# Optimization experiments

Measured on AMD Instinct MI355X. Metric: run time of the kernel, lower is better.

## Reference

```python
import jax, jax.numpy as jnp
import numpy as np

B, T, C, H = 2, 2048, 1024, 16


def setup_inputs() -> dict:
    key = jax.random.key(0)
    ks = jax.random.split(key, 9)
    s = 1.0 / np.sqrt(C)
    return {
        "query": jax.random.normal(ks[0], (B, T, C), dtype=jnp.float32),
        "Wq": jax.random.normal(ks[1], (C, C), dtype=jnp.float32) * s,
        "bq": jnp.zeros((C,), dtype=jnp.float32),
        "Wk": jax.random.normal(ks[2], (C, C), dtype=jnp.float32) * s,
        "bk": jnp.zeros((C,), dtype=jnp.float32),
        "Wv": jax.random.normal(ks[3], (C, C), dtype=jnp.float32) * s,
        "bv": jnp.zeros((C,), dtype=jnp.float32),
        "Wp": jax.random.normal(ks[4], (C, C), dtype=jnp.float32) * s,
        "bp": jnp.zeros((C,), dtype=jnp.float32),
        "n_head": H,
    }


def reference(query, Wq, bq, Wk, bk, Wv, bv, Wp, bp, n_head):
    b, t, c = query.shape
    d = c // n_head
    # QKV projections -> [b, h, t, d]
    q = (query @ Wq + bq).reshape(b, t, n_head, d).transpose(0, 2, 1, 3)
    k = (query @ Wk + bk).reshape(b, t, n_head, d).transpose(0, 2, 1, 3)
    v = (query @ Wv + bv).reshape(b, t, n_head, d).transpose(0, 2, 1, 3)
    scale = 1.0 / jnp.sqrt(jnp.asarray(d, dtype=query.dtype))
    att = jnp.einsum('bhtd,bhsd->bhts', q, k) * scale  # [b,h,t,t]
    causal = jnp.tril(jnp.ones((t, t), dtype=bool))
    att = jnp.where(causal[None, None, :, :], att, -jnp.inf)
    att = jax.nn.softmax(att, axis=-1)
    y = jnp.einsum('bhts,bhsd->bhtd', att, v)  # [b,h,t,d]
    y = y.transpose(0, 2, 1, 3).reshape(b, t, c)
    return y @ Wp + bp
```

## Files before the change

### kernel.cpp

```cpp
#include <hip/hip_runtime.h>
#include <math.h>

#define B_ 2
#define T_ 2048
#define C_ 1024
#define H_ 16
#define D_ 64
#define M_ (B_*T_)

typedef __bf16 bf16x8 __attribute__((ext_vector_type(8)));
typedef __bf16 bf16x4 __attribute__((ext_vector_type(4)));
typedef float  f32x4  __attribute__((ext_vector_type(4)));
typedef float  f32x16 __attribute__((ext_vector_type(16)));

__device__ __forceinline__ unsigned short f2bf(float f) {
    unsigned int u = __float_as_uint(f);
    u += 0x7FFFu + ((u >> 16) & 1u);
    return (unsigned short)(u >> 16);
}

__device__ __forceinline__ bf16x8 pack4(unsigned a, unsigned b,
                                        unsigned c, unsigned d) {
    union { unsigned u[4]; bf16x8 v; } t;
    t.u[0] = a; t.u[1] = b; t.u[2] = c; t.u[3] = d;
    return t.v;
}

__device__ __forceinline__ void gload16(const void* g, void* l) {
    __builtin_amdgcn_global_load_lds(
        (const __attribute__((address_space(1))) void*)g,
        (__attribute__((address_space(3))) void*)l, 16, 0, 0);
}

__global__ __launch_bounds__(256) void prep_kernel(
    const float* __restrict__ X, unsigned short* __restrict__ Xb,
    const float* __restrict__ W0, const float* __restrict__ W1,
    const float* __restrict__ W2, const float* __restrict__ W3,
    unsigned short* __restrict__ T0, unsigned short* __restrict__ T1,
    unsigned short* __restrict__ T2, unsigned short* __restrict__ T3)
{
    const int tid = threadIdx.x;
    if (blockIdx.x < 2048) {
        const size_t i = ((size_t)blockIdx.x * 256 + tid) * 8;
        const float4 a = *(const float4*)&X[i];
        const float4 b = *(const float4*)&X[i + 4];
        ushort4 s0, s1;
        s0.x = f2bf(a.x); s0.y = f2bf(a.y); s0.z = f2bf(a.z); s0.w = f2bf(a.w);
        s1.x = f2bf(b.x); s1.y = f2bf(b.y); s1.z = f2bf(b.z); s1.w = f2bf(b.w);
        *(ushort4*)&Xb[i]     = s0;
        *(ushort4*)&Xb[i + 4] = s1;
        return;
    }
    const int bz = blockIdx.x - 2048;
    const int z = bz >> 10, rem = bz & 1023;
    const float* W; unsigned short* Wt;
    switch (z) {
        case 0: W = W0; Wt = T0; break;
        case 1: W = W1; Wt = T1; break;
        case 2: W = W2; Wt = T2; break;
        default: W = W3; Wt = T3; break;
    }
    __shared__ unsigned short tile[32][33];
    const int k0 = (rem >> 5) * 32, n0 = (rem & 31) * 32;
    {
        const int r = tid >> 3, c = (tid & 7) * 4;
        const float4 v = *(const float4*)&W[(size_t)(k0 + r)*C_ + n0 + c];
        tile[c+0][r] = f2bf(v.x);
        tile[c+1][r] = f2bf(v.y);
        tile[c+2][r] = f2bf(v.z);
        tile[c+3][r] = f2bf(v.w);
    }
    __syncthreads();
    {
        const int r = tid >> 3, c = (tid & 7) * 4;
        ushort4 s;
        s.x = tile[r][c+0]; s.y = tile[r][c+1]; s.z = tile[r][c+2]; s.w = tile[r][c+3];
        *(ushort4*)&Wt[(size_t)(n0 + r)*C_ + k0 + c] = s;
    }
}

__global__ __launch_bounds__(256) void gemm_proj_kernel(
    const unsigned short* __restrict__ A, const unsigned short* __restrict__ Bt,
    const float* __restrict__ bias, float* __restrict__ out)
{
    __shared__ __align__(16) unsigned short lds[4 * 6144];

    const int tid  = threadIdx.x;
    const int lane = tid & 63;
    const int wave = tid >> 6;
    const int wm = wave >> 1, wn = wave & 1;
    const int l15 = lane & 15, quad = lane >> 4;
    const int m0 = blockIdx.y * 64, n0 = blockIdx.x * 128;

    const int lrow = lane >> 2;
    const int csw  = ((lane & 3) ^ ((lane >> 3) & 3)) * 8;
    const int sw8  = (quad ^ ((l15 >> 1) & 3)) * 8;

#define PSTAGE(tt) do {                                                        \
        const int bi_ = ((tt) & 3) * 6144;                                     \
        const int k0_ = (tt) << 5;                                             \
        gload16(&A [(size_t)(m0 + wave*16 + lrow)*C_ + k0_ + csw],             \
                &lds[bi_ + wave*512]);                                         \
        gload16(&Bt[(size_t)(n0 + wave*32 + lrow)*C_ + k0_ + csw],             \
                &lds[bi_ + 2048 + wave*1024]);                                 \
        gload16(&Bt[(size_t)(n0 + wave*32 + 16 + lrow)*C_ + k0_ + csw],        \
                &lds[bi_ + 2048 + wave*1024 + 512]);                           \
    } while (0)

    const f32x4 zero4 = {0.f, 0.f, 0.f, 0.f};
    f32x4 acc[2][4];
    #pragma unroll
    for (int i = 0; i < 2; ++i)
        #pragma unroll
        for (int j = 0; j < 4; ++j) acc[i][j] = zero4;

    PSTAGE(0); PSTAGE(1); PSTAGE(2);

    for (int t = 0; t < 32; ++t) {
        const int bi = (t & 3) * 6144;
        __builtin_amdgcn_s_barrier();
        __builtin_amdgcn_sched_barrier(0);
        if (t <= 29) {
            asm volatile("s_waitcnt vmcnt(6)" ::: "memory");
        } else if (t == 30) {
            asm volatile("s_waitcnt vmcnt(3)" ::: "memory");
        } else {
            asm volatile("s_waitcnt vmcnt(0)" ::: "memory");
        }
        __builtin_amdgcn_s_barrier();
        __builtin_amdgcn_sched_barrier(0);

        const unsigned short* Ab = &lds[bi];
        const unsigned short* Bb = &lds[bi + 2048];

        bf16x8 af[2], bfr[4];
        #pragma unroll
        for (int i = 0; i < 2; ++i)
            af[i] = *(const bf16x8*)&Ab[(wm*32 + i*16 + l15)*32 + sw8];
        #pragma unroll
        for (int j = 0; j < 4; ++j)
            bfr[j] = *(const bf16x8*)&Bb[(wn*64 + j*16 + l15)*32 + sw8];

        if (t < 29) PSTAGE(t + 3);

        __builtin_amdgcn_s_setprio(1);
        #pragma unroll
        for (int i = 0; i < 2; ++i)
            #pragma unroll
            for (int j = 0; j < 4; ++j)
                acc[i][j] = __builtin_amdgcn_mfma_f32_16x16x32_bf16(
                    af[i], bfr[j], acc[i][j], 0, 0, 0);
        __builtin_amdgcn_s_setprio(0);
    }
#undef PSTAGE

    #pragma unroll
    for (int j = 0; j < 4; ++j) {
        const int n = n0 + wn*64 + j*16 + l15;
        const float bv = bias[n];
        #pragma unroll
        for (int i = 0; i < 2; ++i)
            #pragma unroll
            for (int r = 0; r < 4; ++r) {
                const int m = m0 + wm*32 + i*16 + quad*4 + r;
                out[(size_t)m*C_ + n] = acc[i][j][r] + bv;
            }
    }
}

__global__ __launch_bounds__(512, 2) void gemm256_qkv_kernel(
    const unsigned short* __restrict__ A, const unsigned short* __restrict__ Bt,
    const float* __restrict__ b0, const float* __restrict__ b1,
    const float* __restrict__ b2,
    unsigned short* __restrict__ outq, unsigned short* __restrict__ outk,
    unsigned short* __restrict__ outv)
{
    __shared__ __align__(16) unsigned short lds[4 * 16384];

    const int tid  = threadIdx.x;
    const int lane = tid & 63;
    const int wave = tid >> 6;
    const int l15  = lane & 15, quad = lane >> 4;
    const int wm   = wave >> 2, wn = wave & 3;
    const int bid  = blockIdx.y * 12 + blockIdx.x;
    const int swz  = (bid & 7) * 24 + (bid >> 3);
    const int m0   = (swz / 12) * 256, n0 = (swz % 12) * 256;

    const int lrow = lane >> 2;
    const int csw  = ((lane & 3) ^ ((lane >> 3) & 3)) * 8;
    const int sw8  = (quad ^ ((l15 >> 1) & 3)) * 8;

#define STAGE_H(tt, h) do {                                                    \
        const int bi_ = ((tt) & 3) << 14;                                      \
        const int k0_ = (tt) << 5;                                             \
        const int ra_ = m0 + wave*32 + (h)*16 + lrow;                          \
        const int rb_ = n0 + wave*32 + (h)*16 + lrow;                          \
        gload16(&A [(size_t)ra_*C_ + k0_ + csw],                               \
                &lds[bi_ + wave*1024 + (h)*512]);                              \
        gload16(&Bt[(size_t)rb_*C_ + k0_ + csw],                               \
                &lds[bi_ + 8192 + wave*1024 + (h)*512]);                       \
    } while (0)

    const f32x4 zero4 = {0.f, 0.f, 0.f, 0.f};
    f32x4 acc[8][4];
    #pragma unroll
    for (int i = 0; i < 8; ++i)
        #pragma unroll
        for (int j = 0; j < 4; ++j) acc[i][j] = zero4;

    STAGE_H(0,0); STAGE_H(0,1);
    STAGE_H(1,0); STAGE_H(1,1);
    STAGE_H(2,0); STAGE_H(2,1);

    for (int t = 0; t < 32; ++t) {
        const int bi = (t & 3) << 14;
        __builtin_amdgcn_s_barrier();
        __builtin_amdgcn_sched_barrier(0);
        if (t <= 29) {
            asm volatile("s_waitcnt vmcnt(8)" ::: "memory");
        } else if (t == 30) {
            asm volatile("s_waitcnt vmcnt(4)" ::: "memory");
        } else {
            asm volatile("s_waitcnt vmcnt(0)" ::: "memory");
        }
        __builtin_amdgcn_s_barrier();
        __builtin_amdgcn_sched_barrier(0);

        const unsigned short* Ab = &lds[bi];
        const unsigned short* Bb = &lds[bi + 8192];

        bf16x8 bfr[4], af[4];
        #pragma unroll
        for (int j = 0; j < 4; ++j)
            bfr[j] = *(const bf16x8*)&Bb[(wn*64 + j*16 + l15)*32 + sw8];
        #pragma unroll
        for (int i = 0; i < 4; ++i)
            af[i] = *(const bf16x8*)&Ab[(wm*128 + i*16 + l15)*32 + sw8];

        if (t < 29) STAGE_H(t + 3, 0);

        __builtin_amdgcn_s_setprio(1);
        #pragma unroll
        for (int i = 0; i < 4; ++i)
            #pragma unroll
            for (int j = 0; j < 4; ++j)
                acc[i][j] = __builtin_amdgcn_mfma_f32_16x16x32_bf16(
                    af[i], bfr[j], acc[i][j], 0, 0, 0);
        __builtin_amdgcn_s_setprio(0);

        __builtin_amdgcn_s_barrier();
        __builtin_amdgcn_sched_barrier(0);

        #pragma unroll
        for (int i = 0; i < 4; ++i)
            af[i] = *(const bf16x8*)&Ab[(wm*128 + 64 + i*16 + l15)*32 + sw8];

        if (t < 29) STAGE_H(t + 3, 1);

        __builtin_amdgcn_s_setprio(1);
        #pragma unroll
        for (int i = 0; i < 4; ++i)
            #pragma unroll
            for (int j = 0; j < 4; ++j)
                acc[4+i][j] = __builtin_amdgcn_mfma_f32_16x16x32_bf16(
                    af[i], bfr[j], acc[4+i][j], 0, 0, 0);
        __builtin_amdgcn_s_setprio(0);
    }
#undef STAGE_H

    __syncthreads();

    unsigned short* Ep = &lds[wave * 8192];
    const int which = n0 >> 10;
    const int c0 = (n0 & 1023) + wn * 64;
    const int h  = c0 >> 6;
    const int bb = m0 >> 11;
    const int t0 = (m0 & (T_ - 1)) + wm * 128;
    const int bh = bb * H_ + h;
    const float* bp = (which == 0) ? b0 : (which == 1 ? b1 : b2);
    const float qscale = (which == 0) ? 0.18033688f : 1.0f;

    if (which < 2) {
        __bf16* Eb = (__bf16*)Ep;
        #pragma unroll
        for (int j = 0; j < 4; ++j) {
            const int cl = j*16 + l15;
            const float bias = bp[c0 + cl];
            #pragma unroll
            for (int i = 0; i < 8; ++i)
                #pragma unroll
                for (int r = 0; r < 4; ++r)
                    Eb[(i*16 + quad*4 + r)*64 + cl] =
                        (__bf16)((acc[i][j][r] + bias) * qscale);
        }
        unsigned short* op = (which == 0) ? outq : outk;
        const int row8 = lane >> 3, chunk = lane & 7;
        #pragma unroll
        for (int u = 0; u < 16; ++u) {
            const int row = u*8 + row8;
            const uint4 v = *(const uint4*)&Ep[row*64 + chunk*8];
            *(uint4*)&op[((size_t)bh*T_ + t0 + row)*D_ + chunk*8] = v;
        }
    } else {
        #pragma unroll
        for (int j = 0; j < 4; ++j) {
            const int cl = j*16 + l15;
            const float bias = bp[c0 + cl];
            const int xo = (cl & 7) * 8;
            #pragma unroll
            for (int i = 0; i < 8; ++i) {
                bf16x4 pk = {(__bf16)(acc[i][j][0] + bias),
                             (__bf16)(acc[i][j][1] + bias),
                             (__bf16)(acc[i][j][2] + bias),
                             (__bf16)(acc[i][j][3] + bias)};
                *(bf16x4*)&Ep[cl*128 + ((i*16 + quad*4) ^ xo)] = pk;
            }
        }
        const int d4 = lane >> 4, chunk = lane & 15;
        #pragma unroll
        for (int u = 0; u < 16; ++u) {
            const int d = u*4 + d4;
            const uint4 v = *(const uint4*)&Ep[d*128 + ((chunk*8) ^ ((d & 7)*8))];
            *(uint4*)&outv[((size_t)bh*D_ + d)*T_ + t0 + chunk*8] = v;
        }
    }
}

__global__ __launch_bounds__(256) void flash_mfma_kernel(
    const unsigned short* __restrict__ Qs, const unsigned short* __restrict__ Ks,
    const unsigned short* __restrict__ Vts, unsigned short* __restrict__ Y,
    float* __restrict__ parts, float* __restrict__ lbase)
{
    __shared__ __align__(16) unsigned short Kls[64 * 64];
    __shared__ __align__(16) unsigned short Vls[64 * 64];
    __shared__ float lsums[4][32];

    const int tid  = threadIdx.x;
    const int lane = tid & 63, wave = tid >> 6;
    const int krl  = lane & 31, hi = lane >> 5;
    const int srow8 = lane >> 3;
    const int schk8 = ((lane & 7) ^ srow8) * 8;
    const int job  = blockIdx.x >> 5;
    const int bh   = blockIdx.x & 31;
    const bool isA = (job < 8);
    const int a    = isA ? job : job - 8;

    int qts[2], slos[2], shis[2], slots[2], nseg;
    if (isA) {
        qts[0] = a;      slos[0] = 0;        shis[0] = 2*a + 2;  slots[0] = -1;
        qts[1] = 15 - a; slos[1] = 0;        shis[1] = 15 - 2*a; slots[1] = 0;
        nseg = 2;
    } else {
        qts[0] = 15 - a; slos[0] = 15 - 2*a; shis[0] = 32 - 2*a; slots[0] = 1;
        nseg = 1;
    }

    const int b_ = bh >> 4, h_ = bh & (H_ - 1);

#define FSTAGE(itv) do {                                                       \
        const int s0_ = (itv) * 64;                                            \
        const int cu0_ = 2*wave, cu1_ = 2*wave + 1;                            \
        const int r0_ = cu0_*8 + srow8, r1_ = cu1_*8 + srow8;                  \
        gload16(&Ks [((size_t)bh*T_ + s0_ + r0_)*D_ + schk8],                  \
                (char*)Kls + cu0_*1024);                                       \
        gload16(&Vts[((size_t)bh*D_ + r0_)*T_ + s0_ + schk8],                  \
                (char*)Vls + cu0_*1024);                                       \
        gload16(&Ks [((size_t)bh*T_ + s0_ + r1_)*D_ + schk8],                  \
                (char*)Kls + cu1_*1024);                                       \
        gload16(&Vts[((size_t)bh*D_ + r1_)*T_ + s0_ + schk8],                  \
                (char*)Vls + cu1_*1024);                                       \
    } while (0)

    for (int sg = 0; sg < nseg; ++sg) {
        const int qt  = qts[sg];
        const int qw0 = qt * 128 + wave * 32;
        const int qrow = qw0 + krl;

        bf16x8 qf[4];
        #pragma unroll
        for (int ds = 0; ds < 4; ++ds)
            qf[ds] = *(const bf16x8*)&Qs[((size_t)bh*T_ + qrow)*D_ + ds*16 + hi*8];

        f32x16 o[2];
        #pragma unroll
        for (int dt = 0; dt < 2; ++dt)
            #pragma unroll
            for (int r = 0; r < 16; ++r) o[dt][r] = 0.f;
        float lsum = 0.f;

        for (int it = slos[sg]; it < shis[sg]; ++it) {
            const int s0 = it * 64;
            __syncthreads();
            FSTAGE(it);
            __syncthreads();

            if (s0 > qw0 + 31) continue;

            f32x16 st[2];
            #pragma unroll
            for (int kt = 0; kt < 2; ++kt)
                #pragma unroll
                for (int r = 0; r < 16; ++r) st[kt][r] = 0.f;
            #pragma unroll
            for (int kt = 0; kt < 2; ++kt) {
                #pragma unroll
                for (int ds = 0; ds < 4; ++ds) {
                    const int row = kt*32 + krl;
                    bf16x8 kf = *(const bf16x8*)
                        &Kls[row*64 + (((ds*2 + hi) ^ (krl & 7)) << 3)];
                    st[kt] = __builtin_amdgcn_mfma_f32_32x32x16_bf16(
                        kf, qf[ds], st[kt], 0, 0, 0);
                }
            }

            const bool diag = (s0 + 63 > qw0);
            #pragma unroll
            for (int kt = 0; kt < 2; ++kt) {
                const int kb = s0 + kt*32 + 4*hi;
                #pragma unroll
                for (int reg = 0; reg < 16; ++reg) {
                    const int crow = (reg & 3) + 8*(reg >> 2);
                    float e = __builtin_amdgcn_exp2f(st[kt][reg]);
                    if (diag && (kb + crow > qrow)) e = 0.f;
                    st[kt][reg] = e;
                    lsum += e;
                }
            }

            bf16x8 pa[4];
            #pragma unroll
            for (int kt = 0; kt < 2; ++kt) {
                #pragma unroll
                for (int hh = 0; hh < 2; ++hh) {
                    const int rb = hh * 8;
                    unsigned c0, c1, c2, c3;
                    asm("v_cvt_pk_bf16_f32 %0, %1, %2"
                        : "=v"(c0) : "v"(st[kt][rb+0]), "v"(st[kt][rb+1]));
                    asm("v_cvt_pk_bf16_f32 %0, %1, %2"
                        : "=v"(c1) : "v"(st[kt][rb+2]), "v"(st[kt][rb+3]));
                    asm("v_cvt_pk_bf16_f32 %0, %1, %2"
                        : "=v"(c2) : "v"(st[kt][rb+4]), "v"(st[kt][rb+5]));
                    asm("v_cvt_pk_bf16_f32 %0, %1, %2"
                        : "=v"(c3) : "v"(st[kt][rb+6]), "v"(st[kt][rb+7]));
                    asm("v_permlane32_swap_b32 %0, %1" : "+v"(c0), "+v"(c2));
                    asm("v_permlane32_swap_b32 %0, %1" : "+v"(c1), "+v"(c3));
                    pa[kt*2 + hh] = pack4(c0, c1, c2, c3);
                }
            }

            #pragma unroll
            for (int dt = 0; dt < 2; ++dt) {
                #pragma unroll
                for (int ks = 0; ks < 4; ++ks) {
                    const int rowd = dt*32 + krl;
                    bf16x8 vb = *(const bf16x8*)
                        &Vls[rowd*64 + (((ks*2 + hi) ^ (krl & 7)) << 3)];
                    o[dt] = __builtin_amdgcn_mfma_f32_32x32x16_bf16(
                        pa[ks], vb, o[dt], 0, 0, 0);
                }
            }
        }

        lsum += __shfl_xor(lsum, 32, 64);
        if (lane < 32) lsums[wave][krl] = lsum;

        if (slots[sg] < 0) {
            #pragma unroll
            for (int reg = 0; reg < 16; ++reg) {
                const int q = (reg & 3) + 8*(reg >> 2) + 4*hi;
                const float inv = 1.0f / lsums[wave][q];
                const size_t yb = ((size_t)(b_*T_ + qw0 + q))*C_ + h_*D_;
                *(__bf16*)&Y[yb + krl]      = (__bf16)(o[0][reg] * inv);
                *(__bf16*)&Y[yb + 32 + krl] = (__bf16)(o[1][reg] * inv);
            }
        } else {
            const int gpi = bh*16 + a*2 + slots[sg];
            float* Op = parts + (size_t)gpi*8192;
            float* Lp = lbase + gpi*128;
            if (lane < 32) Lp[wave*32 + lane] = lsum;
            #pragma unroll
            for (int reg = 0; reg < 16; ++reg) {
                const int tl = wave*32 + (reg & 3) + 8*(reg >> 2) + 4*hi;
                Op[(size_t)tl*64 + krl]      = o[0][reg];
                Op[(size_t)tl*64 + 32 + krl] = o[1][reg];
            }
        }
    }
#undef FSTAGE
}

__global__ __launch_bounds__(256) void merge_kernel(
    const float* __restrict__ parts, const float* __restrict__ lbase,
    unsigned short* __restrict__ Y)
{
    const int pair = blockIdx.x;
    const int bh = pair >> 3, p = pair & 7;
    const int qt = 15 - p;
    const int g0 = bh*16 + p*2;
    const float* O0 = parts + (size_t)g0*8192;
    const float* O1 = O0 + 8192;
    const float* L0 = lbase + g0*128;
    const float* L1 = L0 + 128;

    const int tid = threadIdx.x;
    const int r = tid >> 1, c0 = (tid & 1) * 32;
    const float inv = 1.0f / (L0[r] + L1[r]);
    const int b = bh >> 4, h = bh & (H_ - 1);
    const int t = qt*128 + r;
    #pragma unroll
    for (int k = 0; k < 8; ++k) {
        const f32x4 a  = *(const f32x4*)&O0[(size_t)r*64 + c0 + k*4];
        const f32x4 bb = *(const f32x4*)&O1[(size_t)r*64 + c0 + k*4];
        bf16x4 pk = {(__bf16)((a[0]+bb[0])*inv), (__bf16)((a[1]+bb[1])*inv),
                     (__bf16)((a[2]+bb[2])*inv), (__bf16)((a[3]+bb[3])*inv)};
        *(bf16x4*)&Y[((size_t)(b*T_ + t))*C_ + h*D_ + c0 + k*4] = pk;
    }
}

extern "C" void kernel_launch(void* const* d_in, const int* in_sizes, int n_in,
                              void* d_out, int out_size, void* d_ws, size_t ws_size,
                              hipStream_t stream) {
    const float* query = (const float*)d_in[0];
    const float* Wq = (const float*)d_in[1];
    const float* bq = (const float*)d_in[2];
    const float* Wk = (const float*)d_in[3];
    const float* bk = (const float*)d_in[4];
    const float* Wv = (const float*)d_in[5];
    const float* bv = (const float*)d_in[6];
    const float* Wp = (const float*)d_in[7];
    const float* bp = (const float*)d_in[8];
    float* out = (float*)d_out;

    char* ws = (char*)d_ws;
    unsigned short* qbf   = (unsigned short*)(ws);
    unsigned short* kbf   = (unsigned short*)(ws + 8388608);
    unsigned short* vtbf  = (unsigned short*)(ws + 16777216);
    unsigned short* WtP   = (unsigned short*)(ws + 25165824);
    unsigned short* WtQKV = (unsigned short*)(ws + 27262976);
    unsigned short* yb    = (unsigned short*)(ws + 33554432);
    unsigned short* qx    = (unsigned short*)(ws + 41943040);
    float* lbase = (float*)(ws + 27262976);
    float* parts = out;

    prep_kernel<<<6144, 256, 0, stream>>>(
        query, qx, Wq, Wk, Wv, Wp,
        WtQKV, WtQKV + (size_t)C_*C_, WtQKV + 2*(size_t)C_*C_, WtP);

    gemm256_qkv_kernel<<<dim3(12, 16), 512, 0, stream>>>(
        qx, WtQKV, bq, bk, bv, qbf, kbf, vtbf);

    flash_mfma_kernel<<<512, 256, 0, stream>>>(qbf, kbf, vtbf, yb, parts, lbase);
    merge_kernel<<<256, 256, 0, stream>>>(parts, lbase, yb);

    gemm_proj_kernel<<<dim3(C_/128, M_/64), 256, 0, stream>>>(
        yb, WtP, bp, out);
}
```

Measured before the change: 187.6 us.

## Halve QKV GEMM LDS to double buffering and split epilogue in two halves

Cuts the QKV projection GEMM's LDS staging from four buffers to two (prefetch distance 1 instead of 3) and raises the launch-bounds hint to 4 blocks per CU. The epilogue is split into two half passes so it fits the smaller 4096-element per-wave LDS scratch. The aim is more resident blocks per CU to hide latency, at the cost of a shallower prefetch pipeline with a full vmcnt(0) wait every iteration. The tighter register budget may also cause spills given the 32 f32x4 accumulators per thread.

```diff
diff --git a/kernel.cpp b/kernel.cpp
--- a/kernel.cpp
+++ b/kernel.cpp
@@ -168,14 +168,14 @@
     }
 }
 
-__global__ __launch_bounds__(512, 2) void gemm256_qkv_kernel(
+__global__ __launch_bounds__(512, 4) void gemm256_qkv_kernel(
     const unsigned short* __restrict__ A, const unsigned short* __restrict__ Bt,
     const float* __restrict__ b0, const float* __restrict__ b1,
     const float* __restrict__ b2,
     unsigned short* __restrict__ outq, unsigned short* __restrict__ outk,
     unsigned short* __restrict__ outv)
 {
-    __shared__ __align__(16) unsigned short lds[4 * 16384];
+    __shared__ __align__(16) unsigned short lds[2 * 16384];
 
     const int tid  = threadIdx.x;
     const int lane = tid & 63;
@@ -191,7 +191,7 @@
     const int sw8  = (quad ^ ((l15 >> 1) & 3)) * 8;
 
 #define STAGE_H(tt, h) do {                                                    \
-        const int bi_ = ((tt) & 3) << 14;                                      \
+        const int bi_ = ((tt) & 1) << 14;                                      \
         const int k0_ = (tt) << 5;                                             \
         const int ra_ = m0 + wave*32 + (h)*16 + lrow;                          \
         const int rb_ = n0 + wave*32 + (h)*16 + lrow;                          \
@@ -209,20 +209,12 @@
         for (int j = 0; j < 4; ++j) acc[i][j] = zero4;
 
     STAGE_H(0,0); STAGE_H(0,1);
-    STAGE_H(1,0); STAGE_H(1,1);
-    STAGE_H(2,0); STAGE_H(2,1);
 
     for (int t = 0; t < 32; ++t) {
-        const int bi = (t & 3) << 14;
+        const int bi = (t & 1) << 14;
         __builtin_amdgcn_s_barrier();
         __builtin_amdgcn_sched_barrier(0);
-        if (t <= 29) {
-            asm volatile("s_waitcnt vmcnt(8)" ::: "memory");
-        } else if (t == 30) {
-            asm volatile("s_waitcnt vmcnt(4)" ::: "memory");
-        } else {
-            asm volatile("s_waitcnt vmcnt(0)" ::: "memory");
-        }
+        asm volatile("s_waitcnt vmcnt(0)" ::: "memory");
         __builtin_amdgcn_s_barrier();
         __builtin_amdgcn_sched_barrier(0);
 
@@ -237,7 +229,7 @@
         for (int i = 0; i < 4; ++i)
             af[i] = *(const bf16x8*)&Ab[(wm*128 + i*16 + l15)*32 + sw8];
 
-        if (t < 29) STAGE_H(t + 3, 0);
+        if (t < 31) STAGE_H(t + 1, 0);
 
         __builtin_amdgcn_s_setprio(1);
         #pragma unroll
@@ -255,7 +247,7 @@
         for (int i = 0; i < 4; ++i)
             af[i] = *(const bf16x8*)&Ab[(wm*128 + 64 + i*16 + l15)*32 + sw8];
 
-        if (t < 29) STAGE_H(t + 3, 1);
+        if (t < 31) STAGE_H(t + 1, 1);
 
         __builtin_amdgcn_s_setprio(1);
         #pragma unroll
@@ -270,7 +262,7 @@
 
     __syncthreads();
 
-    unsigned short* Ep = &lds[wave * 8192];
+    unsigned short* Ep = &lds[wave * 4096];
     const int which = n0 >> 10;
     const int c0 = (n0 & 1023) + wn * 64;
     const int h  = c0 >> 6;
@@ -281,47 +273,55 @@
     const float qscale = (which == 0) ? 0.18033688f : 1.0f;
 
     if (which < 2) {
+        unsigned short* op = (which == 0) ? outq : outk;
         __bf16* Eb = (__bf16*)Ep;
-        #pragma unroll
-        for (int j = 0; j < 4; ++j) {
-            const int cl = j*16 + l15;
-            const float bias = bp[c0 + cl];
-            #pragma unroll
-            for (int i = 0; i < 8; ++i)
-                #pragma unroll
-                for (int r = 0; r < 4; ++r)
-                    Eb[(i*16 + quad*4 + r)*64 + cl] =
-                        (__bf16)((acc[i][j][r] + bias) * qscale);
-        }
-        unsigned short* op = (which == 0) ? outq : outk;
         const int row8 = lane >> 3, chunk = lane & 7;
         #pragma unroll
-        for (int u = 0; u < 16; ++u) {
-            const int row = u*8 + row8;
-            const uint4 v = *(const uint4*)&Ep[row*64 + chunk*8];
-            *(uint4*)&op[((size_t)bh*T_ + t0 + row)*D_ + chunk*8] = v;
+        for (int hb = 0; hb < 2; ++hb) {
+            #pragma unroll
+            for (int j = 0; j < 4; ++j) {
+                const int cl = j*16 + l15;
+                const float bias = bp[c0 + cl];
+                #pragma unroll
+                for (int i = 0; i < 4; ++i)
+                    #pragma unroll
+                    for (int r = 0; r < 4; ++r)
+                        Eb[(i*16 + quad*4 + r)*64 + cl] =
+                            (__bf16)((acc[hb*4 + i][j][r] + bias) * qscale);
+            }
+            #pragma unroll
+            for (int u = 0; u < 8; ++u) {
+                const int row = u*8 + row8;
+                const uint4 v = *(const uint4*)&Ep[row*64 + chunk*8];
+                *(uint4*)&op[((size_t)bh*T_ + t0 + hb*64 + row)*D_ + chunk*8] = v;
+            }
         }
     } else {
-        #pragma unroll
-        for (int j = 0; j < 4; ++j) {
-            const int cl = j*16 + l15;
-            const float bias = bp[c0 + cl];
-            const int xo = (cl & 7) * 8;
-            #pragma unroll
-            for (int i = 0; i < 8; ++i) {
-                bf16x4 pk = {(__bf16)(acc[i][j][0] + bias),
-                             (__bf16)(acc[i][j][1] + bias),
-                             (__bf16)(acc[i][j][2] + bias),
-                             (__bf16)(acc[i][j][3] + bias)};
-                *(bf16x4*)&Ep[cl*128 + ((i*16 + quad*4) ^ xo)] = pk;
-            }
-        }
         const int d4 = lane >> 4, chunk = lane & 15;
         #pragma unroll
-        for (int u = 0; u < 16; ++u) {
-            const int d = u*4 + d4;
-            const uint4 v = *(const uint4*)&Ep[d*128 + ((chunk*8) ^ ((d & 7)*8))];
-            *(uint4*)&outv[((size_t)bh*D_ + d)*T_ + t0 + chunk*8] = v;
+        for (int hb = 0; hb < 2; ++hb) {
+            #pragma unroll
+            for (int j = 0; j < 2; ++j) {
+                const int cl = (hb*2 + j)*16 + l15;
+                const float bias = bp[c0 + cl];
+                const int lcl = cl - hb*32;
+                const int xo = (cl & 7) * 8;
+                #pragma unroll
+                for (int i = 0; i < 8; ++i) {
+                    bf16x4 pk = {(__bf16)(acc[i][hb*2 + j][0] + bias),
+                                 (__bf16)(acc[i][hb*2 + j][1] + bias),
+                                 (__bf16)(acc[i][hb*2 + j][2] + bias),
+                                 (__bf16)(acc[i][hb*2 + j][3] + bias)};
+                    *(bf16x4*)&Ep[lcl*128 + ((i*16 + quad*4) ^ xo)] = pk;
+                }
+            }
+            #pragma unroll
+            for (int u = 0; u < 8; ++u) {
+                const int d = hb*32 + u*4 + d4;
+                const uint4 v = *(const uint4*)
+                    &Ep[(d - hb*32)*128 + ((chunk*8) ^ ((d & 7)*8))];
+                *(uint4*)&outv[((size_t)bh*D_ + d)*T_ + t0 + chunk*8] = v;
+            }
         }
     }
 }
```

After: 368.0 us. 1.96x slower.
